# Performance work log

Measured on AMD Instinct MI355X. Metric: run time of the kernel, lower is better.

## Reference

```python
import jax, jax.numpy as jnp
import numpy as np

B, T, C = 2, 1024, 1024
HS = 64
H = C // HS                 # 16 wkv heads
C_ATT = 512
H_GQA = C_ATT // HS         # 8 kv heads
GROUP = H // H_GQA          # 2
D_DECAY, D_AAA, D_MV, D_GATE = 64, 64, 32, 160


def setup_inputs() -> dict:
    key = jax.random.key(0)
    ks = jax.random.split(key, 16)
    f32 = jnp.float32
    rn = lambda k, shp, s=0.02: jax.random.normal(k, shp, dtype=f32) * s
    return {
        'x': jax.random.normal(ks[0], (B, T, C), f32),
        'wkv_state_in': jnp.zeros((B, H, HS, HS), f32),
        'v_first_val': jax.random.normal(ks[1], (B, T, C), f32),
        'w0': jnp.linspace(-6.5, -1.5, C, dtype=f32).reshape(1, 1, C) + 0.5,
        'w1': rn(ks[2], (C, D_DECAY)), 'w2': rn(ks[3], (D_DECAY, C)),
        'a0': jnp.zeros((1, 1, C), f32),
        'a1': rn(ks[4], (C, D_AAA)), 'a2': rn(ks[5], (D_AAA, C)),
        'v0': jnp.ones((1, 1, C), f32),
        'v1': rn(ks[6], (C, D_MV)), 'v2': rn(ks[7], (D_MV, C)),
        'g1': rn(ks[8], (C, D_GATE)), 'g2': rn(ks[9], (D_GATE, C)),
        'k_k': jnp.full((1, 1, C), 0.85, f32),
        'k_a': jnp.ones((1, 1, C), f32),
        'r_k': rn(ks[10], (H, HS)),
        'Wq': rn(ks[11], (C, C)), 'Wk': rn(ks[12], (C_ATT, C)),
        'Wv': rn(ks[13], (C_ATT, C)), 'Wo': rn(ks[14], (C, C)),
        'ln_w': jnp.ones((C,), f32), 'ln_b': jnp.zeros((C,), f32),
    }


def _gqa_expand(t):
    # [B,T,C_ATT] -> repeat each kv head GROUP times -> [B,T,C]
    t = t.reshape(B, T, H_GQA, 1, HS)
    return jnp.broadcast_to(t, (B, T, H_GQA, GROUP, HS)).reshape(B, T, C)


def _wkv_scan(r, decay, k, v, a, b, S0):
    # all seq tensors [B,T,H,N]; scan over time with state S [B,H,N,N]
    seq = tuple(x.transpose(1, 0, 2, 3) for x in (r, decay, k, v, a, b))

    def step(S, ins):
        r_t, w_t, k_t, v_t, a_t, b_t = ins  # [B,H,N]
        sa = jnp.einsum('bhij,bhj->bhi', S, a_t)
        S = (S * w_t[:, :, None, :]
             + sa[..., None] * b_t[:, :, None, :]
             + v_t[..., None] * k_t[:, :, None, :])
        y = jnp.einsum('bhij,bhj->bhi', S, r_t)
        return S, y

    S_out, ys = jax.lax.scan(step, S0, seq)
    return ys.transpose(1, 0, 2, 3), S_out  # [B,T,H,N], [B,H,N,N]


def _forward(x, wkv_state_in, v_first_val, w0, w1, w2, a0, a1, a2, v0, v1, v2,
             g1, g2, k_k, k_a, r_k, Wq, Wk, Wv, Wo, ln_w, ln_b):
    r = x @ Wq.T                                   # [B,T,C]
    w = w0 + jnp.tanh(x @ w1) @ w2                 # decay logits [B,T,C]
    k = _gqa_expand(x @ Wk.T)                      # [B,T,C]
    v = _gqa_expand(x @ Wv.T)
    g = jax.nn.sigmoid(x @ g1) @ g2                # gate
    iclr = jax.nn.sigmoid(a0 + (x @ a1) @ a2)      # in-context learning rate

    kk = (k * k_k).reshape(B, T, H, HS)
    kk = kk / jnp.maximum(jnp.linalg.norm(kk, axis=-1, keepdims=True), 1e-12)
    kk = kk.reshape(B, T, C)

    iclr = 1.0 + (iclr - 1.0) * k_a
    k = k * iclr
    # layer_id > 0: mix v toward v_first
    v = v + (v_first_val - v) * jax.nn.sigmoid(v0 + (x @ v1) @ v2)

    decay = jnp.exp(-jnp.exp(w))                   # per-channel decay in (0,1)
    hv = lambda t: t.reshape(B, T, H, HS)
    xx, S_out = _wkv_scan(hv(r), hv(decay), hv(k), hv(v), hv(-kk), hv(kk * iclr), wkv_state_in)

    # GroupNorm with n_head groups, eps = 1e-5 * head_size
    mu = xx.mean(-1, keepdims=True)
    var = xx.var(-1, keepdims=True)
    xn = (xx - mu) * jax.lax.rsqrt(var + 1e-5 * HS)
    xn = xn.reshape(B, T, C) * ln_w + ln_b

    # r_k bonus term (standard RWKV7 epilogue)
    bonus = ((hv(r) * hv(k) * r_k).sum(-1, keepdims=True) * hv(v)).reshape(B, T, C)
    xn = xn + bonus

    out = (xn * g) @ Wo.T
    return out, S_out, v_first_val


def reference(x, wkv_state_in, v_first_val, w0, w1, w2, a0, a1, a2, v0, v1, v2,
              g1, g2, k_k, k_a, r_k, Wq, Wk, Wv, Wo, ln_w, ln_b):
    return _forward(x, wkv_state_in, v_first_val, w0, w1, w2, a0, a1, a2,
                    v0, v1, v2, g1, g2, k_k, k_a, r_k, Wq, Wk, Wv, Wo, ln_w, ln_b)
```

## Files before the change

### kernel.cpp

```cpp
#include <hip/hip_runtime.h>

typedef unsigned short u16;
typedef __attribute__((ext_vector_type(8))) short s16x8;
typedef __attribute__((ext_vector_type(4))) float f32x4;
typedef __attribute__((ext_vector_type(4))) int   i32x4;
typedef __attribute__((ext_vector_type(2))) int   i32x2;
typedef __attribute__((ext_vector_type(4))) unsigned short u16x4;

constexpr size_t OFF_XB   = 0;
constexpr size_t OFF_WQB  = OFF_XB   + 4194304;
constexpr size_t OFF_WKB  = OFF_WQB  + 2097152;
constexpr size_t OFF_WVB  = OFF_WKB  + 1048576;
constexpr size_t OFF_WOB  = OFF_WVB  + 1048576;
constexpr size_t OFF_W1T  = OFF_WOB  + 2097152;
constexpr size_t OFF_W2T  = OFF_W1T  + 786432;
constexpr size_t OFF_A2T  = OFF_W2T  + 131072;
constexpr size_t OFF_V2T  = OFF_A2T  + 131072;
constexpr size_t OFF_G2T  = OFF_V2T  + 65536;
constexpr size_t OFF_KQF  = OFF_G2T  + 327680;
constexpr size_t OFF_VQF  = OFF_KQF  + 4194304;
constexpr size_t OFF_URAW = OFF_VQF  + 4194304;
constexpr size_t OFF_UB   = OFF_URAW + 2621440;
constexpr size_t OFF_S2A  = OFF_UB   + 1572864;
constexpr size_t OFF_S2V  = OFF_S2A  + 8388608;
constexpr size_t OFF_GBUF = OFF_S2V  + 8388608;
constexpr size_t OFF_SEQ  = OFF_GBUF + 8388608;
constexpr size_t OFF_YBUF = OFF_SEQ  + 50331648;
constexpr size_t OFF_XGB  = OFF_YBUF + 8388608;

constexpr size_t OFF_VEPI = OFF_XB;
constexpr size_t OFF_DP   = OFF_W1T;

__device__ __forceinline__ u16 f2bf(float f){
  unsigned int u = __builtin_bit_cast(unsigned int, f);
  u = u + 0x7fffu + ((u >> 16) & 1u);
  return (u16)(u >> 16);
}
__device__ __forceinline__ int pk2(float a, float b){
  return (int)((unsigned)f2bf(a) | ((unsigned)f2bf(b) << 16));
}
__device__ __forceinline__ int cvtpk(float a, float b){
  int r;
  asm("v_cvt_pk_bf16_f32 %0, %1, %2" : "=v"(r) : "v"(a), "v"(b));
  return r;
}
__device__ __forceinline__ float bf2f(u16 h){
  return __builtin_bit_cast(float, ((unsigned)h) << 16);
}
__device__ __forceinline__ f32x4 cvt4(i32x2 v){
  unsigned a=(unsigned)v[0], b=(unsigned)v[1];
  f32x4 r;
  r[0]=__builtin_bit_cast(float, a<<16);
  r[1]=__builtin_bit_cast(float, a&0xffff0000u);
  r[2]=__builtin_bit_cast(float, b<<16);
  r[3]=__builtin_bit_cast(float, b&0xffff0000u);
  return r;
}

__device__ __forceinline__ void gload_lds16(const float* g, float* l){
  __builtin_amdgcn_global_load_lds((const __attribute__((address_space(1))) void*)g,
                                   (__attribute__((address_space(3))) void*)l, 16, 0, 0);
}
__device__ __forceinline__ void gload_lds16u(const u16* g, u16* l){
  __builtin_amdgcn_global_load_lds((const __attribute__((address_space(1))) void*)g,
                                   (__attribute__((address_space(3))) void*)l, 16, 0, 0);
}
__device__ __forceinline__ void gload_lds4(const float* g, float* l){
  __builtin_amdgcn_global_load_lds((const __attribute__((address_space(1))) void*)g,
                                   (__attribute__((address_space(3))) void*)l, 4, 0, 0);
}

constexpr size_t N_XB=2097152, N_WQ=1048576, N_WK=524288, N_WV=524288, N_WO=1048576,
  N_W1T=393216, N_W2T=65536, N_A2T=65536, N_V2T=32768, N_G2T=163840, N_VF=2097152;
constexpr size_t PREP_TOT = N_XB+N_WQ+N_WK+N_WV+N_WO+N_W1T+N_W2T+N_A2T+N_V2T+N_G2T+N_VF;

__global__ __launch_bounds__(256) void prep_kernel(char* ws, const float* x, const float* vfirst,
  const float* w1, const float* w2, const float* a1, const float* a2,
  const float* v1, const float* v2, const float* g1, const float* g2,
  const float* Wq, const float* Wk, const float* Wv, const float* Wo, float* dout)
{
  u16* XB=(u16*)(ws+OFF_XB); u16* WQB=(u16*)(ws+OFF_WQB); u16* WKB=(u16*)(ws+OFF_WKB);
  u16* WVB=(u16*)(ws+OFF_WVB); u16* WOB=(u16*)(ws+OFF_WOB); u16* W1T=(u16*)(ws+OFF_W1T);
  u16* W2T=(u16*)(ws+OFF_W2T); u16* A2T=(u16*)(ws+OFF_A2T); u16* V2T=(u16*)(ws+OFF_V2T);
  u16* G2T=(u16*)(ws+OFF_G2T);
  for (size_t idx=(size_t)blockIdx.x*256+threadIdx.x; idx<PREP_TOT; idx+=(size_t)gridDim.x*256){
    size_t r = idx;
    if (r < N_XB){ XB[r]=f2bf(x[r]); continue; } r-=N_XB;
    if (r < N_WQ){ WQB[r]=f2bf(Wq[r]); continue; } r-=N_WQ;
    if (r < N_WK){ WKB[r]=f2bf(Wk[r]); continue; } r-=N_WK;
    if (r < N_WV){ WVB[r]=f2bf(Wv[r]); continue; } r-=N_WV;
    if (r < N_WO){ WOB[r]=f2bf(Wo[r]); continue; } r-=N_WO;
    if (r < N_W1T){
      int n=(int)(r>>10), k=(int)(r&1023); float v=0.f;
      if (n<64) v=w1[(size_t)k*64+n];
      else if (n<128) v=a1[(size_t)k*64+(n-64)];
      else if (n<160) v=v1[(size_t)k*32+(n-128)];
      else if (n<320) v=g1[(size_t)k*160+(n-160)];
      W1T[r]=f2bf(v); continue; } r-=N_W1T;
    if (r < N_W2T){ int c=(int)(r>>6), d=(int)(r&63); W2T[r]=f2bf(w2[(size_t)d*1024+c]); continue; } r-=N_W2T;
    if (r < N_A2T){ int c=(int)(r>>6), d=(int)(r&63); A2T[r]=f2bf(a2[(size_t)d*1024+c]); continue; } r-=N_A2T;
    if (r < N_V2T){ int c=(int)(r>>5), d=(int)(r&31); V2T[r]=f2bf(v2[(size_t)d*1024+c]); continue; } r-=N_V2T;
    if (r < N_G2T){ int c=(int)(r/160), d=(int)(r%160); G2T[r]=f2bf(g2[(size_t)d*1024+c]); continue; } r-=N_G2T;
    dout[2228224 + r] = vfirst[r];
  }
}

__global__ __launch_bounds__(256) void gemm_kernel(int phase, char* ws,
  const float* w0b, const float* a0b, const float* v0b, float* dout)
{
  const u16* A; const u16* Bw;
  float* outF=nullptr; const float* bias=nullptr;
  char* SEQc=(char*)(ws+OFF_SEQ);
  u16* UBp=(u16*)(ws+OFF_UB);
  int lda=0, ldb=0, K=0, ldc=0, Nlim=1024, col0=0, outMode=0;
  int y = blockIdx.y;
  if (phase==0){
    A=(const u16*)(ws+OFF_XB); lda=1024; K=1024;
    if (y<8)      { Bw=(const u16*)(ws+OFF_WQB); ldb=1024; col0=y*128;       outMode=1; }
    else if (y<12){ Bw=(const u16*)(ws+OFF_WKB); ldb=1024; col0=(y-8)*128;   outF=(float*)(ws+OFF_KQF); ldc=512; Nlim=512; }
    else if (y<16){ Bw=(const u16*)(ws+OFF_WVB); ldb=1024; col0=(y-12)*128;  outF=(float*)(ws+OFF_VQF); ldc=512; Nlim=512; }
    else          { Bw=(const u16*)(ws+OFF_W1T); ldb=1024; col0=(y-16)*128;  outMode=4; Nlim=320; }
  } else if (phase==1){
    int seg=y>>3; col0=(y&7)*128;
    const int Ks[4]={64,64,32,160};
    const int Ao[4]={0,64,128,160};
    K=Ks[seg]; lda=384; ldb=K;
    A=(const u16*)(ws+OFF_UB) + Ao[seg];
    if (seg==0)     { Bw=(const u16*)(ws+OFF_W2T); outMode=2; bias=w0b; }
    else if (seg==1){ Bw=(const u16*)(ws+OFF_A2T); outMode=3; bias=a0b; outF=(float*)(ws+OFF_S2A); ldc=1024; }
    else if (seg==2){ Bw=(const u16*)(ws+OFF_V2T); outMode=3; bias=v0b; outF=(float*)(ws+OFF_S2V); ldc=1024; }
    else            { Bw=(const u16*)(ws+OFF_G2T); outF=(float*)(ws+OFF_GBUF); ldc=1024; }
  } else {
    A=(const u16*)(ws+OFF_XGB); lda=1024; K=1024;
    Bw=(const u16*)(ws+OFF_WOB); ldb=1024; col0=y*128; outF=dout; ldc=1024;
  }
  int m0 = blockIdx.x*64;
  __shared__ __align__(16) u16 As[2][2048];
  __shared__ __align__(16) u16 Bs[2][4096];
  int tid=threadIdx.x, l=tid&63, wv=tid>>6, wm=wv>>1, wn=wv&1;

  int cswz = (l&3) ^ ((l>>3)&3);
  int srA = wv*16 + (l>>2);
  int srB = wv*32 + (l>>2);
  const u16* aP0 = A  + (size_t)(m0+srA)*lda       + cswz*8;
  const u16* bP0 = Bw + (size_t)(col0+srB)*ldb     + cswz*8;
  const u16* bP1 = Bw + (size_t)(col0+srB+16)*ldb  + cswz*8;

  f32x4 acc[2][4];
  #pragma unroll
  for (int i=0;i<2;i++)
    #pragma unroll
    for (int j=0;j<4;j++) acc[i][j]=(f32x4){0.f,0.f,0.f,0.f};

#define GSTAGE(b,k0) do{                                   \
    gload_lds16u(aP0 + (k0), &As[b][wv*512]);              \
    gload_lds16u(bP0 + (k0), &Bs[b][wv*1024]);             \
    gload_lds16u(bP1 + (k0), &Bs[b][wv*1024+512]);         \
  }while(0)

  GSTAGE(0,0);
  asm volatile("s_waitcnt vmcnt(0)" ::: "memory");
  __syncthreads();

  int rrow=l&15, ck=l>>4;
  for (int k0=0;k0<K;k0+=32){
    int cb=(k0>>5)&1;
    if (k0+32<K) GSTAGE(cb^1, k0+32);
    s16x8 af[2], bf[4];
    #pragma unroll
    for (int mt=0;mt<2;mt++){
      int ra = wm*32+mt*16+rrow;
      af[mt]=*(const s16x8*)(&As[cb][ra*32 + ((ck ^ ((ra>>1)&3))<<3)]);
    }
    #pragma unroll
    for (int nt=0;nt<4;nt++){
      int rb = wn*64+nt*16+rrow;
      bf[nt]=*(const s16x8*)(&Bs[cb][rb*32 + ((ck ^ ((rb>>1)&3))<<3)]);
    }
    #pragma unroll
    for (int mt=0;mt<2;mt++)
      #pragma unroll
      for (int nt=0;nt<4;nt++)
        acc[mt][nt]=__builtin_amdgcn_mfma_f32_16x16x32_bf16(af[mt],bf[nt],acc[mt][nt],0,0,0);
    __syncthreads();
  }
#undef GSTAGE
  #pragma unroll
  for (int mt=0;mt<2;mt++){
    #pragma unroll
    for (int nt=0;nt<4;nt++){
      int nglob = col0 + wn*64 + nt*16 + (l&15);
      if (nglob >= Nlim) continue;
      #pragma unroll
      for (int rg=0;rg<4;rg++){
        int mrow = m0 + wm*32 + mt*16 + ((l>>4)<<2) + rg;
        float val = acc[mt][nt][rg];
        if (outMode==0){
          outF[(size_t)mrow*ldc + nglob] = val;
        } else if (outMode==1){
          int b=mrow>>10, t=mrow&1023, h=nglob>>6, i=nglob&63;
          char* cbase = SEQc + (size_t)((b*16+h)*64 + (t>>4))*24576 + (size_t)(t&15)*896;
          *(u16*)(cbase + i*2) = f2bf(val);
        } else if (outMode==2){
          float w = bias[nglob] + val;
          float d = expf(-expf(w));
          int b=mrow>>10, t=mrow&1023, h=nglob>>6, i=nglob&63;
          char* cbase = SEQc + (size_t)((b*16+h)*64 + (t>>4))*24576 + (size_t)(t&15)*896;
          *(float*)(cbase + 640 + i*4) = d;
        } else if (outMode==3){
          float s = 1.0f/(1.0f+__expf(-(bias[nglob]+val)));
          outF[(size_t)mrow*ldc + nglob] = s;
        } else {
          float a = (nglob<64) ? tanhf(val)
                  : (nglob<160) ? val
                  : 1.0f/(1.0f+__expf(-val));
          UBp[(size_t)mrow*384 + nglob] = f2bf(a);
        }
      }
    }
  }
}

__global__ __launch_bounds__(256) void prep2_kernel(char* ws, const float* vfirst,
  const float* kk_s, const float* ka_s, const float* rkw)
{
  const float* KQF=(const float*)(ws+OFF_KQF);
  const float* VQF=(const float*)(ws+OFF_VQF);
  const float* ICLR=(const float*)(ws+OFF_S2A);
  const float* VMIX=(const float*)(ws+OFF_S2V);
  u16* VEPI=(u16*)(ws+OFF_VEPI);
  float* DPp=(float*)(ws+OFF_DP);
  int m=blockIdx.x, b=m>>10, t=m&1023;
  int tid=threadIdx.x, c0=tid*4, h=c0>>6, i0=c0&63, hk=h>>1;
  f32x4 kq=*(const f32x4*)(KQF+(size_t)m*512+hk*64+i0);
  f32x4 vq=*(const f32x4*)(VQF+(size_t)m*512+hk*64+i0);
  f32x4 ic=*(const f32x4*)(ICLR+(size_t)m*1024+c0);
  f32x4 vm=*(const f32x4*)(VMIX+(size_t)m*1024+c0);
  f32x4 vf=*(const f32x4*)(vfirst+(size_t)m*1024+c0);
  f32x4 kkc=*(const f32x4*)(kk_s+c0);
  f32x4 kac=*(const f32x4*)(ka_s+c0);
  f32x4 kk=kq*kkc;
  float ssq=kk[0]*kk[0]+kk[1]*kk[1]+kk[2]*kk[2]+kk[3]*kk[3];
  #pragma unroll
  for (int mk=1;mk<16;mk<<=1) ssq += __shfl_xor(ssq,mk);
  float scale = 1.0f / fmaxf(sqrtf(ssq), 1e-12f);
  int bh=b*16+h;
  char* cb = ws + OFF_SEQ + (size_t)(bh*64+(t>>4))*24576 + (size_t)(t&15)*896;
  u16x4 rv = *(const u16x4*)(cb + (size_t)i0*2);
  f32x4 rkv = *(const f32x4*)(rkw + h*64 + i0);
  f32x4 kf,vv,av,bv;
  float dpp=0.f;
  #pragma unroll
  for (int j=0;j<4;j++){
    float icc = 1.0f + (ic[j]-1.0f)*kac[j];
    float kkn = kk[j]*scale;
    kf[j]=kq[j]*icc;
    vv[j]=vq[j] + (vf[j]-vq[j])*vm[j];
    av[j]=-kkn;
    bv[j]=kkn*icc;
    dpp += bf2f(rv[j])*kf[j]*rkv[j];
  }
  #pragma unroll
  for (int mk=1;mk<16;mk<<=1) dpp += __shfl_xor(dpp,mk);
  if ((tid&15)==0) DPp[(size_t)bh*1024 + t] = dpp;
  i32x2 o;
  o[0]=pk2(kf[0],kf[1]); o[1]=pk2(kf[2],kf[3]);
  *(i32x2*)(cb + 128 + (size_t)i0*2) = o;
  o[0]=pk2(vv[0],vv[1]); o[1]=pk2(vv[2],vv[3]);
  *(i32x2*)(cb + 256 + (size_t)i0*2) = o;
  *(i32x2*)(VEPI + ((size_t)bh*1024+t)*64 + i0) = o;
  o[0]=pk2(av[0],av[1]); o[1]=pk2(av[2],av[3]);
  *(i32x2*)(cb + 384 + (size_t)i0*2) = o;
  o[0]=pk2(bv[0],bv[1]); o[1]=pk2(bv[2],bv[3]);
  *(i32x2*)(cb + 512 + (size_t)i0*2) = o;
}

#define MFMA32(a,b,c) __builtin_amdgcn_mfma_f32_16x16x32_bf16(a,b,c,0,0,0)

__global__ __launch_bounds__(64) void pre_kernel(char* ws){
  int bid=blockIdx.x;
  int l=threadIdx.x, c16=l&15, g=l>>4;
  char* chunk = ws + OFF_SEQ + (size_t)bid*24576;
  char* rec = chunk;

  __shared__ __align__(16) char SH[31776];
  u16* AT =(u16*)(SH+14336);
  u16* RT =(u16*)(SH+16640);
  u16* BT =(u16*)(SH+18944);
  u16* KT =(u16*)(SH+21248);
  u16* vbb=(u16*)(SH+23552);
  u16* BKL=(u16*)(SH+26656);
  float* WN  =(float*)(SH+0);
  u16* WY =(u16*)(SH+1088);
  u16* WB =(u16*)(SH+1888);
  u16* WK =(u16*)(SH+2688);
  u16* pbb=(u16*)(SH+3488);
  u16* zbb=(u16*)(SH+6592);
  float* rhsb=(float*)(SH+9696);
  float* gtmp=(float*)(SH+9696);
  const s16x8 zero8 = {0,0,0,0,0,0,0,0};
  const f32x4 zf4 = {0.f,0.f,0.f,0.f};

  #pragma unroll
  for (int q=0;q<14;q++)
    gload_lds16((const float*)(chunk + (size_t)q*1024) + l*4, (float*)(SH + q*1024));
  asm volatile("s_waitcnt vmcnt(0)" ::: "memory");
  __builtin_amdgcn_sched_barrier(0);

  float ptv[16]; float pp=1.f;
  #pragma unroll
  for (int t=0;t<16;t++){ pp *= *(const float*)(SH + t*896 + 640 + l*4); ptv[t]=pp; }
  float pL = ptv[15];
  *(float*)(rec + 10240 + (size_t)l*4) = pL;
  float rpL = __builtin_amdgcn_rcpf(pL);
  float bs[16], ks[16];
  u16 vcol[16];
  #pragma unroll
  for (int t=0;t<16;t++){
    float sc = pL * __builtin_amdgcn_rcpf(ptv[t]);
    bs[t] = bf2f(*(const u16*)(SH + t*896 + 512 + l*2)) * sc;
    ks[t] = bf2f(*(const u16*)(SH + t*896 + 128 + l*2)) * sc;
    vcol[t] = *(const u16*)(SH + t*896 + 256 + l*2);
  }
  {
    i32x4 o;
    o[0]=(int)((unsigned)vcol[0]|((unsigned)vcol[1]<<16));
    o[1]=(int)((unsigned)vcol[2]|((unsigned)vcol[3]<<16));
    o[2]=(int)((unsigned)vcol[4]|((unsigned)vcol[5]<<16));
    o[3]=(int)((unsigned)vcol[6]|((unsigned)vcol[7]<<16));
    *(i32x4*)(&vbb[l*24]) = o;
    o[0]=(int)((unsigned)vcol[8]|((unsigned)vcol[9]<<16));
    o[1]=(int)((unsigned)vcol[10]|((unsigned)vcol[11]<<16));
    o[2]=(int)((unsigned)vcol[12]|((unsigned)vcol[13]<<16));
    o[3]=(int)((unsigned)vcol[14]|((unsigned)vcol[15]<<16));
    *(i32x4*)(&vbb[l*24+8]) = o;
    o[0]=pk2(bs[0],bs[1]); o[1]=pk2(bs[2],bs[3]); o[2]=pk2(bs[4],bs[5]); o[3]=pk2(bs[6],bs[7]);
    *(i32x4*)(&BKL[l*40]) = o;
    o[0]=pk2(bs[8],bs[9]); o[1]=pk2(bs[10],bs[11]); o[2]=pk2(bs[12],bs[13]); o[3]=pk2(bs[14],bs[15]);
    *(i32x4*)(&BKL[l*40+8]) = o;
    o[0]=pk2(ks[0],ks[1]); o[1]=pk2(ks[2],ks[3]); o[2]=pk2(ks[4],ks[5]); o[3]=pk2(ks[6],ks[7]);
    *(i32x4*)(&BKL[l*40+16]) = o;
    o[0]=pk2(ks[8],ks[9]); o[1]=pk2(ks[10],ks[11]); o[2]=pk2(ks[12],ks[13]); o[3]=pk2(ks[14],ks[15]);
    *(i32x4*)(&BKL[l*40+24]) = o;
  }
  #pragma unroll
  for (int t=0;t<16;t++){
    float at = bf2f(*(const u16*)(SH + t*896 + 384 + l*2));
    float rt = bf2f(*(const u16*)(SH + t*896 +   0 + l*2));
    float pprev = (t==0) ? 1.f : ptv[t-1];
    AT[t*72+l] = f2bf(pprev*at);
    RT[t*72+l] = f2bf(ptv[t]*rt);
    BT[t*72+l] = f2bf(bs[t]*rpL);
    KT[t*72+l] = f2bf(ks[t]*rpL);
  }
  asm volatile("s_waitcnt lgkmcnt(0)" ::: "memory");
  __builtin_amdgcn_sched_barrier(0);

  {
    s16x8 afA[2], afR[2], bfB[2], bfK[2];
    #pragma unroll
    for (int Kt=0;Kt<2;Kt++){
      afA[Kt]=*(const s16x8*)(&AT[c16*72 + 32*Kt + 8*g]);
      afR[Kt]=*(const s16x8*)(&RT[c16*72 + 32*Kt + 8*g]);
      bfB[Kt]=*(const s16x8*)(&BT[c16*72 + 32*Kt + 8*g]);
      bfK[Kt]=*(const s16x8*)(&KT[c16*72 + 32*Kt + 8*g]);
    }
    f32x4 dNN=zf4, dNY=zf4, dBB=zf4, dBK=zf4;
    #pragma unroll
    for (int Kt=0;Kt<2;Kt++){
      dNN=MFMA32(afA[Kt],bfB[Kt],dNN);
      dNY=MFMA32(afA[Kt],bfK[Kt],dNY);
      dBB=MFMA32(afR[Kt],bfB[Kt],dBB);
      dBK=MFMA32(afR[Kt],bfK[Kt],dBK);
    }
    #pragma unroll
    for (int e=0;e<4;e++){
      int tR=4*g+e, sC=c16;
      WN[tR*17+sC] = dNN[e];
      WY[tR*24+sC] = (sC<tR)? f2bf(dNY[e]) : (u16)0;
      WB[tR*24+sC] = (sC<=tR)? f2bf(dBB[e]) : (u16)0;
      WK[tR*24+sC] = (sC<=tR)? f2bf(dBK[e]) : (u16)0;
    }
  }

  s16x8 vf[4];
  #pragma unroll
  for (int J=0;J<4;J++){
    vf[J]=zero8;
    if (g<2) vf[J]=*(const s16x8*)(&vbb[(16*J+c16)*24 + 8*g]);
  }
  {
    s16x8 wyf=zero8;
    if (g<2) wyf=*(const s16x8*)(&WY[c16*24 + 8*g]);
    f32x4 dR[4];
    #pragma unroll
    for (int J=0;J<4;J++){
      dR[J]=zf4;
      dR[J]=MFMA32(wyf,vf[J],dR[J]);
      #pragma unroll
      for (int e=0;e<4;e++)
        rhsb[(4*g+e)*68 + 16*J + c16] = dR[J][e];
    }
  }

  {
    float pv[16];
    #pragma unroll
    for (int t=0;t<16;t++) pv[t]=bf2f(AT[t*72+l]);
    #pragma unroll
    for (int t=1;t<16;t++)
      #pragma unroll
      for (int s=0;s<16;s++){
        if (s<t) pv[t] += WN[t*17+s]*pv[s];
      }
    i32x4 o;
    o[0]=pk2(pv[0],pv[1]); o[1]=pk2(pv[2],pv[3]); o[2]=pk2(pv[4],pv[5]); o[3]=pk2(pv[6],pv[7]);
    *(i32x4*)(&pbb[l*24]) = o;
    o[0]=pk2(pv[8],pv[9]); o[1]=pk2(pv[10],pv[11]); o[2]=pk2(pv[12],pv[13]); o[3]=pk2(pv[14],pv[15]);
    *(i32x4*)(&pbb[l*24+8]) = o;
  }

  {
    float zz[16];
    #pragma unroll
    for (int t=0;t<16;t++) zz[t]=rhsb[t*68+l];
    #pragma unroll
    for (int t=1;t<16;t++)
      #pragma unroll
      for (int s=0;s<16;s++){
        if (s<t) zz[t] += WN[t*17+s]*zz[s];
      }
    i32x4 o;
    o[0]=pk2(zz[0],zz[1]); o[1]=pk2(zz[2],zz[3]); o[2]=pk2(zz[4],zz[5]); o[3]=pk2(zz[6],zz[7]);
    *(i32x4*)(&zbb[l*24]) = o;
    o[0]=pk2(zz[8],zz[9]); o[1]=pk2(zz[10],zz[11]); o[2]=pk2(zz[12],zz[13]); o[3]=pk2(zz[14],zz[15]);
    *(i32x4*)(&zbb[l*24+8]) = o;
  }
  asm volatile("s_waitcnt lgkmcnt(0)" ::: "memory");
  __builtin_amdgcn_sched_barrier(0);

  {
    s16x8 wbf=zero8, wkf=zero8;
    if (g<2){
      wbf=*(const s16x8*)(&WB[c16*24 + 8*g]);
      wkf=*(const s16x8*)(&WK[c16*24 + 8*g]);
    }
    #pragma unroll
    for (int J=0;J<4;J++){
      s16x8 pfB=zero8, zfB=zero8;
      if (g<2){
        pfB=*(const s16x8*)(&pbb[(16*J+c16)*24 + 8*g]);
        zfB=*(const s16x8*)(&zbb[(16*J+c16)*24 + 8*g]);
      }
      f32x4 dG, dYl=zf4;
      #pragma unroll
      for (int e=0;e<4;e++) dG[e]=bf2f(RT[(4*g+e)*72 + 16*J + c16]);
      dG=MFMA32(wbf,pfB,dG);
      dYl=MFMA32(wbf,zfB,dYl);
      dYl=MFMA32(wkf,vf[J],dYl);
      #pragma unroll
      for (int e=0;e<4;e++) gtmp[(4*g+e)*68 + 16*J + c16]=dG[e];
      i32x2 o2; o2[0]=pk2(dYl[0],dYl[1]); o2[1]=pk2(dYl[2],dYl[3]);
      *(i32x2*)(rec + 10496 + (size_t)J*2560 + 2048 + (size_t)l*8) = o2;
    }
  }

  {
    s16x8 bk[4], pfr[4], bzv[4];
    #pragma unroll
    for (int nt=0;nt<4;nt++) bk[nt]=*(const s16x8*)(&BKL[(16*nt+c16)*40 + 8*g]);
    #pragma unroll
    for (int mt=0;mt<4;mt++)
      pfr[mt]= (g<2) ? *(const s16x8*)(&pbb[(16*mt+c16)*24 + 8*g]) : zero8;
    #pragma unroll
    for (int it=0;it<4;it++)
      bzv[it]= (g<2) ? *(const s16x8*)(&zbb[(16*it+c16)*24 + 8*g])
                     : *(const s16x8*)(&vbb[(16*it+c16)*24 + 8*(g-2)]);
    #pragma unroll
    for (int mt=0;mt<4;mt++){
      #pragma unroll
      for (int nt=0;nt<4;nt++){
        f32x4 dQ = MFMA32(pfr[mt], bk[nt], zf4);
        int kk = mt>>1, gq = ((mt&1)<<1) | (g>>1), jo = g&1;
        i32x2 o2; o2[0]=pk2(dQ[0],dQ[1]); o2[1]=pk2(dQ[2],dQ[3]);
        *(i32x2*)(rec + ((size_t)(kk*4+nt)*64 + (size_t)(c16 + 16*gq))*16 + 8*jo) = o2;
      }
    }
    #pragma unroll
    for (int jtp=0;jtp<4;jtp++){
      #pragma unroll
      for (int it=0;it<4;it++){
        f32x4 dc = MFMA32(bk[jtp], bzv[it], zf4);
        i32x2 o2; o2[0]=pk2(dc[0],dc[1]); o2[1]=pk2(dc[2],dc[3]);
        *(i32x2*)(rec + 10496 + (size_t)it*2560 + ((size_t)jtp*64 + l)*8) = o2;
      }
    }
  }

  #pragma unroll
  for (int kk=0;kk<2;kk++){
    f32x4 b0 = *(const f32x4*)(&gtmp[c16*68 + 32*kk + 8*g]);
    f32x4 b1 = *(const f32x4*)(&gtmp[c16*68 + 32*kk + 8*g + 4]);
    i32x4 o;
    o[0]=pk2(b0[0],b0[1]); o[1]=pk2(b0[2],b0[3]); o[2]=pk2(b1[0],b1[1]); o[3]=pk2(b1[2],b1[3]);
    *(i32x4*)(rec + 8192 + (size_t)(kk*64+l)*16) = o;
  }
}

__global__ __launch_bounds__(64) void scan2_kernel(char* ws, const float* S0, float* dout){
  float* YB=(float*)(ws+OFF_YBUF);
  const char* recb = ws + OFF_SEQ;
  int bid=blockIdx.x, bh=bid>>2, w=bid&3;
  int l=threadIdx.x, c16=l&15, g=l>>4;

  __shared__ __align__(16) u16 ST[16*88];

  f32x4 Sreg[4];
  #pragma unroll
  for (int jt=0;jt<4;jt++)
    Sreg[jt] = *(const f32x4*)(S0 + (size_t)bh*4096 + (size_t)(16*w+c16)*64 + 16*jt + 4*g);
  #pragma unroll
  for (int jt=0;jt<4;jt++){
    i32x2 p; p[0]=pk2(Sreg[jt][0],Sreg[jt][1]); p[1]=pk2(Sreg[jt][2],Sreg[jt][3]);
    *(i32x2*)(&ST[c16*88 + 16*jt + 4*g]) = p;
  }

  const char* rb = recb + (size_t)(bh*64)*24576;
  float* yb0 = YB + (size_t)bh*65536;

#define DECLR(S) s16x8 qf##S[8]; s16x8 gf##S[2]; f32x4 pl##S[4]; i32x2 cf##S[4]; i32x2 yl##S;
#define LOADR(S, nc) do{ \
    const char* rp_ = rb + (size_t)(nc)*24576; \
    _Pragma("unroll") \
    for (int q_=0;q_<8;q_++) qf##S[q_] = *(const s16x8*)(rp_ + (size_t)q_*1024 + l*16); \
    gf##S[0] = *(const s16x8*)(rp_ + 8192 + (size_t)l*16); \
    gf##S[1] = *(const s16x8*)(rp_ + 9216 + (size_t)l*16); \
    _Pragma("unroll") \
    for (int jt_=0;jt_<4;jt_++) pl##S[jt_] = *(const f32x4*)(rp_ + 10240 + (size_t)(16*jt_+4*g)*4); \
    _Pragma("unroll") \
    for (int jt_=0;jt_<4;jt_++) cf##S[jt_] = *(const i32x2*)(rp_ + 10496 + (size_t)w*2560 + (size_t)(jt_*64+l)*8); \
    yl##S = *(const i32x2*)(rp_ + 10496 + (size_t)w*2560 + 2048 + (size_t)l*8); \
  }while(0)
#define STEP(S, ch) do{ \
    s16x8 sB0=*(const s16x8*)(&ST[c16*88 + 8*g]); \
    s16x8 sB1=*(const s16x8*)(&ST[c16*88 + 32 + 8*g]); \
    f32x4 dy=cvt4(yl##S); \
    dy=MFMA32(gf##S[0],sB0,dy); dy=MFMA32(gf##S[1],sB1,dy); \
    _Pragma("unroll") \
    for (int jt_=0;jt_<4;jt_++){ \
      f32x4 acc = cvt4(cf##S[jt_]); \
      acc = MFMA32(qf##S[jt_], sB0, acc); \
      acc = MFMA32(qf##S[4+jt_], sB1, acc); \
      _Pragma("unroll") \
      for (int e_=0;e_<4;e_++) acc[e_] = fmaf(pl##S[jt_][e_], Sreg[jt_][e_], acc[e_]); \
      Sreg[jt_]=acc; \
    } \
    _Pragma("unroll") \
    for (int jt_=0;jt_<4;jt_++){ \
      i32x2 p_; p_[0]=cvtpk(Sreg[jt_][0],Sreg[jt_][1]); p_[1]=cvtpk(Sreg[jt_][2],Sreg[jt_][3]); \
      *(i32x2*)(&ST[c16*88 + 16*jt_ + 4*g]) = p_; \
    } \
    { float* yb_ = yb0 + (size_t)(ch)*1024; \
      _Pragma("unroll") \
      for (int e_=0;e_<4;e_++) yb_[(size_t)(4*g+e_)*64 + 16*w + c16] = dy[e_]; } \
  }while(0)

  DECLR(A); DECLR(B);
  LOADR(A, 0);
  LOADR(B, 1);

  #pragma unroll 1
  for (int ch=0; ch<64; ch+=2){
    STEP(A, ch);
    { int nc = ch+2; if (nc>63) nc=63; LOADR(A, nc); }
    STEP(B, ch+1);
    { int nc = ch+3; if (nc>63) nc=63; LOADR(B, nc); }
  }
#undef DECLR
#undef LOADR
#undef STEP

  #pragma unroll
  for (int jt=0;jt<4;jt++)
    *(f32x4*)(dout + 2097152 + (size_t)bh*4096 + (size_t)(16*w+c16)*64 + 16*jt + 4*g) = Sreg[jt];
}

__global__ __launch_bounds__(256) void epi_kernel(char* ws, const float* lnw, const float* lnb)
{
  const float* YB=(const float*)(ws+OFF_YBUF);
  const u16* VEPI=(const u16*)(ws+OFF_VEPI);
  const float* DPp=(const float*)(ws+OFF_DP);
  const float* GB=(const float*)(ws+OFF_GBUF);
  u16* XGB=(u16*)(ws+OFF_XGB);
  int m=blockIdx.x, b=m>>10, t=m&1023;
  int tid=threadIdx.x, c0=tid*4, h=c0>>6, i0=c0&63;
  f32x4 y=*(const f32x4*)(YB + ((size_t)(b*16+h)*1024+t)*64 + i0);
  float s = y[0]+y[1]+y[2]+y[3];
  float ss= y[0]*y[0]+y[1]*y[1]+y[2]*y[2]+y[3]*y[3];
  #pragma unroll
  for (int mk=1;mk<16;mk<<=1){ s+=__shfl_xor(s,mk); ss+=__shfl_xor(ss,mk); }
  float mu=s*(1.0f/64.0f), var=ss*(1.0f/64.0f)-mu*mu;
  float inv=rsqrtf(var + 6.4e-4f);
  u16x4 v16=*(const u16x4*)(VEPI + ((size_t)(b*16+h)*1024+t)*64 + i0);
  float dp = DPp[(size_t)(b*16+h)*1024 + t];
  f32x4 gg=*(const f32x4*)(GB+(size_t)m*1024+c0);
  u16x4 outv;
  #pragma unroll
  for (int j=0;j<4;j++){
    float xn = (y[j]-mu)*inv*lnw[c0+j] + lnb[c0+j] + dp*bf2f(v16[j]);
    outv[j]=f2bf(xn*gg[j]);
  }
  *(u16x4*)(XGB+(size_t)m*1024+c0)=outv;
}

extern "C" void kernel_launch(void* const* d_in, const int* in_sizes, int n_in,
                              void* d_out, int out_size, void* d_ws, size_t ws_size,
                              hipStream_t stream) {
  const float* x      =(const float*)d_in[0];
  const float* S0     =(const float*)d_in[1];
  const float* vfirst =(const float*)d_in[2];
  const float* w0     =(const float*)d_in[3];
  const float* w1     =(const float*)d_in[4];
  const float* w2     =(const float*)d_in[5];
  const float* a0     =(const float*)d_in[6];
  const float* a1     =(const float*)d_in[7];
  const float* a2     =(const float*)d_in[8];
  const float* v0     =(const float*)d_in[9];
  const float* v1     =(const float*)d_in[10];
  const float* v2     =(const float*)d_in[11];
  const float* g1     =(const float*)d_in[12];
  const float* g2     =(const float*)d_in[13];
  const float* k_k    =(const float*)d_in[14];
  const float* k_a    =(const float*)d_in[15];
  const float* r_k    =(const float*)d_in[16];
  const float* Wq     =(const float*)d_in[17];
  const float* Wk     =(const float*)d_in[18];
  const float* Wv     =(const float*)d_in[19];
  const float* Wo     =(const float*)d_in[20];
  const float* ln_w   =(const float*)d_in[21];
  const float* ln_b   =(const float*)d_in[22];
  char* ws=(char*)d_ws;
  float* dout=(float*)d_out;

  prep_kernel<<<2048,256,0,stream>>>(ws,x,vfirst,w1,w2,a1,a2,v1,v2,g1,g2,Wq,Wk,Wv,Wo,dout);
  gemm_kernel<<<dim3(32,19),256,0,stream>>>(0,ws,w0,a0,v0,dout);
  gemm_kernel<<<dim3(32,32),256,0,stream>>>(1,ws,w0,a0,v0,dout);
  prep2_kernel<<<2048,256,0,stream>>>(ws,vfirst,k_k,k_a,r_k);
  pre_kernel<<<2048,64,0,stream>>>(ws);
  scan2_kernel<<<128,64,0,stream>>>(ws,S0,dout);
  epi_kernel<<<2048,256,0,stream>>>(ws,ln_w,ln_b);
  gemm_kernel<<<dim3(32,8),256,0,stream>>>(2,ws,w0,a0,v0,dout);
}
```

Before: 159.5 us.

## Vectorize prep conversions and merge scan waves into single 256-thread blocks

The prep kernel now converts the bulk fp32 tensors (x, Wq, Wk, Wv, Wo) and copies v_first four elements per thread using 16-byte loads, instead of one scalar element per thread. This cuts instruction count and memory transactions for the largest part of the preprocessing. The scan kernel is reorganised from 128 single-wave blocks into 32 blocks of four waves, one block per batch-head, each wave with its own LDS state tile. That lets the four waves of a head share a CU and its cache for the per-chunk record reads, but uses fewer blocks and so may spread the scan over fewer CUs.

Result: no change. 159.3 us (-0.1%).

```diff
diff --git a/kernel.cpp b/kernel.cpp
--- a/kernel.cpp
+++ b/kernel.cpp
@@ -65,14 +65,13 @@
   __builtin_amdgcn_global_load_lds((const __attribute__((address_space(1))) void*)g,
                                    (__attribute__((address_space(3))) void*)l, 16, 0, 0);
 }
-__device__ __forceinline__ void gload_lds4(const float* g, float* l){
-  __builtin_amdgcn_global_load_lds((const __attribute__((address_space(1))) void*)g,
-                                   (__attribute__((address_space(3))) void*)l, 4, 0, 0);
-}
 
 constexpr size_t N_XB=2097152, N_WQ=1048576, N_WK=524288, N_WV=524288, N_WO=1048576,
   N_W1T=393216, N_W2T=65536, N_A2T=65536, N_V2T=32768, N_G2T=163840, N_VF=2097152;
-constexpr size_t PREP_TOT = N_XB+N_WQ+N_WK+N_WV+N_WO+N_W1T+N_W2T+N_A2T+N_V2T+N_G2T+N_VF;
+constexpr size_t NV_BULK = (N_XB+N_WQ+N_WK+N_WV+N_WO)/4;
+constexpr size_t NV_VF   = N_VF/4;
+constexpr size_t N_SCAL  = N_W1T+N_W2T+N_A2T+N_V2T+N_G2T;
+constexpr size_t PREP_TOT = NV_BULK + NV_VF + N_SCAL;
 
 __global__ __launch_bounds__(256) void prep_kernel(char* ws, const float* x, const float* vfirst,
   const float* w1, const float* w2, const float* a1, const float* a2,
@@ -85,11 +84,32 @@
   u16* G2T=(u16*)(ws+OFF_G2T);
   for (size_t idx=(size_t)blockIdx.x*256+threadIdx.x; idx<PREP_TOT; idx+=(size_t)gridDim.x*256){
     size_t r = idx;
-    if (r < N_XB){ XB[r]=f2bf(x[r]); continue; } r-=N_XB;
-    if (r < N_WQ){ WQB[r]=f2bf(Wq[r]); continue; } r-=N_WQ;
-    if (r < N_WK){ WKB[r]=f2bf(Wk[r]); continue; } r-=N_WK;
-    if (r < N_WV){ WVB[r]=f2bf(Wv[r]); continue; } r-=N_WV;
-    if (r < N_WO){ WOB[r]=f2bf(Wo[r]); continue; } r-=N_WO;
+    if (r < NV_BULK){
+      size_t e = r*4;
+      const float* src; u16* dst;
+      if (e < N_XB){ src=x+e; dst=XB+e; }
+      else { e-=N_XB;
+        if (e < N_WQ){ src=Wq+e; dst=WQB+e; }
+        else { e-=N_WQ;
+          if (e < N_WK){ src=Wk+e; dst=WKB+e; }
+          else { e-=N_WK;
+            if (e < N_WV){ src=Wv+e; dst=WVB+e; }
+            else { e-=N_WV; src=Wo+e; dst=WOB+e; }
+          }
+        }
+      }
+      f32x4 v=*(const f32x4*)src;
+      u16x4 o; o[0]=f2bf(v[0]); o[1]=f2bf(v[1]); o[2]=f2bf(v[2]); o[3]=f2bf(v[3]);
+      *(u16x4*)dst=o;
+      continue;
+    }
+    r -= NV_BULK;
+    if (r < NV_VF){
+      size_t e=r*4;
+      *(f32x4*)(dout + 2228224 + e) = *(const f32x4*)(vfirst + e);
+      continue;
+    }
+    r -= NV_VF;
     if (r < N_W1T){
       int n=(int)(r>>10), k=(int)(r&1023); float v=0.f;
       if (n<64) v=w1[(size_t)k*64+n];
@@ -100,8 +120,7 @@
     if (r < N_W2T){ int c=(int)(r>>6), d=(int)(r&63); W2T[r]=f2bf(w2[(size_t)d*1024+c]); continue; } r-=N_W2T;
     if (r < N_A2T){ int c=(int)(r>>6), d=(int)(r&63); A2T[r]=f2bf(a2[(size_t)d*1024+c]); continue; } r-=N_A2T;
     if (r < N_V2T){ int c=(int)(r>>5), d=(int)(r&31); V2T[r]=f2bf(v2[(size_t)d*1024+c]); continue; } r-=N_V2T;
-    if (r < N_G2T){ int c=(int)(r/160), d=(int)(r%160); G2T[r]=f2bf(g2[(size_t)d*1024+c]); continue; } r-=N_G2T;
-    dout[2228224 + r] = vfirst[r];
+    { int c=(int)(r/160), d=(int)(r%160); G2T[r]=f2bf(g2[(size_t)d*1024+c]); }
   }
 }
 
@@ -507,13 +526,14 @@
   }
 }
 
-__global__ __launch_bounds__(64) void scan2_kernel(char* ws, const float* S0, float* dout){
+__global__ __launch_bounds__(256) void scan2_kernel(char* ws, const float* S0, float* dout){
   float* YB=(float*)(ws+OFF_YBUF);
   const char* recb = ws + OFF_SEQ;
-  int bid=blockIdx.x, bh=bid>>2, w=bid&3;
-  int l=threadIdx.x, c16=l&15, g=l>>4;
-
-  __shared__ __align__(16) u16 ST[16*88];
+  int bh=blockIdx.x;
+  int tid=threadIdx.x, w=tid>>6, l=tid&63, c16=l&15, g=l>>4;
+
+  __shared__ __align__(16) u16 ST[4][16*88];
+  u16* STw = &ST[w][0];
 
   f32x4 Sreg[4];
   #pragma unroll
@@ -522,7 +542,7 @@
   #pragma unroll
   for (int jt=0;jt<4;jt++){
     i32x2 p; p[0]=pk2(Sreg[jt][0],Sreg[jt][1]); p[1]=pk2(Sreg[jt][2],Sreg[jt][3]);
-    *(i32x2*)(&ST[c16*88 + 16*jt + 4*g]) = p;
+    *(i32x2*)(&STw[c16*88 + 16*jt + 4*g]) = p;
   }
 
   const char* rb = recb + (size_t)(bh*64)*24576;
@@ -542,8 +562,8 @@
     yl##S = *(const i32x2*)(rp_ + 10496 + (size_t)w*2560 + 2048 + (size_t)l*8); \
   }while(0)
 #define STEP(S, ch) do{ \
-    s16x8 sB0=*(const s16x8*)(&ST[c16*88 + 8*g]); \
-    s16x8 sB1=*(const s16x8*)(&ST[c16*88 + 32 + 8*g]); \
+    s16x8 sB0=*(const s16x8*)(&STw[c16*88 + 8*g]); \
+    s16x8 sB1=*(const s16x8*)(&STw[c16*88 + 32 + 8*g]); \
     f32x4 dy=cvt4(yl##S); \
     dy=MFMA32(gf##S[0],sB0,dy); dy=MFMA32(gf##S[1],sB1,dy); \
     _Pragma("unroll") \
@@ -558,7 +578,7 @@
     _Pragma("unroll") \
     for (int jt_=0;jt_<4;jt_++){ \
       i32x2 p_; p_[0]=cvtpk(Sreg[jt_][0],Sreg[jt_][1]); p_[1]=cvtpk(Sreg[jt_][2],Sreg[jt_][3]); \
-      *(i32x2*)(&ST[c16*88 + 16*jt_ + 4*g]) = p_; \
+      *(i32x2*)(&STw[c16*88 + 16*jt_ + 4*g]) = p_; \
     } \
     { float* yb_ = yb0 + (size_t)(ch)*1024; \
       _Pragma("unroll") \
@@ -647,7 +667,7 @@
   gemm_kernel<<<dim3(32,32),256,0,stream>>>(1,ws,w0,a0,v0,dout);
   prep2_kernel<<<2048,256,0,stream>>>(ws,vfirst,k_k,k_a,r_k);
   pre_kernel<<<2048,64,0,stream>>>(ws);
-  scan2_kernel<<<128,64,0,stream>>>(ws,S0,dout);
+  scan2_kernel<<<32,256,0,stream>>>(ws,S0,dout);
   epi_kernel<<<2048,256,0,stream>>>(ws,ln_w,ln_b);
   gemm_kernel<<<dim3(32,8),256,0,stream>>>(2,ws,w0,a0,v0,dout);
 }
```
